# Optimization experiments

Hardware: AMD Instinct MI355X
Metric: run time of the kernel (lower is better)

The kernel has to match this reference:

```python
import jax, jax.numpy as jnp
import numpy as np

COMM_DIM = 8
HIDDEN = 64
N = 2048


def setup_inputs() -> dict:
    key = jax.random.key(0)
    k_msg, k_w1, k_b1, k_w2, k_b2 = jax.random.split(key, 5)
    s1 = 1.0 / np.sqrt(2 * COMM_DIM)  # torch Linear default-ish scale
    s2 = 1.0 / np.sqrt(HIDDEN)
    return {
        "messages": jax.random.normal(k_msg, (N, COMM_DIM), dtype=jnp.float32),
        "W1": jax.random.normal(k_w1, (HIDDEN, 2 * COMM_DIM), dtype=jnp.float32) * s1,
        "b1": jax.random.normal(k_b1, (HIDDEN,), dtype=jnp.float32) * s1,
        "W2": jax.random.normal(k_w2, (COMM_DIM, HIDDEN), dtype=jnp.float32) * s2,
        "b2": jax.random.normal(k_b2, (COMM_DIM,), dtype=jnp.float32) * s2,
    }


def reference(messages, W1, b1, W2, b2):
    # edge_mlp(concat([m_i, m_j])) for all ordered pairs, mean over j != i.
    # Linear1 on the concat splits: concat([mi,mj]) @ W1^T = mi @ W1[:,:D]^T + mj @ W1[:,D:]^T
    n = messages.shape[0]
    X1 = jnp.einsum('nd,hd->nh', messages, W1[:, :COMM_DIM])   # [N, H] contribution of m_i
    X2 = jnp.einsum('nd,hd->nh', messages, W1[:, COMM_DIM:])   # [N, H] contribution of m_j
    # pairwise hidden: [N, N, H] (the dominant, memory-bound intermediate)
    H = jax.nn.relu(X1[:, None, :] + X2[None, :, :] + b1)
    S = H.sum(axis=1)                                          # [N, H] sum over all j (incl. j==i)
    D = jax.nn.relu(X1 + X2 + b1)                              # [N, H] the j==i diagonal term
    # agg_i = sum_{j!=i} (relu(...) @ W2^T + b2); then divide by (N-1)
    agg = jnp.einsum('nh,dh->nd', S - D, W2) + (n - 1) * b2
    return agg / (n - 1)
```

## Files before the change

### kernel.cpp

```cpp
#include <hip/hip_runtime.h>


#define NN 2048
#define HH 64
#define DD 8

#define ITILES 32
#define JCHUNKS 32
#define JCHUNK (NN / JCHUNKS)

__global__ void prep_kernel(const float* __restrict__ msg,
                            const float* __restrict__ W1,
                            const float* __restrict__ b1,
                            float* __restrict__ A,
                            float* __restrict__ X2,
                            float* __restrict__ SX) {
    int idx = blockIdx.x * blockDim.x + threadIdx.x;
    if (blockIdx.x == 0 && threadIdx.x < HH) SX[threadIdx.x] = 0.f;
    int i = idx >> 6;
    int h = idx & 63;
    const float4* m4 = (const float4*)(msg + i * DD);
    const float4* w4 = (const float4*)(W1 + h * (2 * DD));
    float4 m0 = m4[0], m1 = m4[1];
    float4 w0 = w4[0], w1 = w4[1], w2 = w4[2], w3 = w4[3];
    float x1 = m0.x * w0.x + m0.y * w0.y + m0.z * w0.z + m0.w * w0.w
             + m1.x * w1.x + m1.y * w1.y + m1.z * w1.z + m1.w * w1.w;
    float x2 = m0.x * w2.x + m0.y * w2.y + m0.z * w2.z + m0.w * w2.w
             + m1.x * w3.x + m1.y * w3.y + m1.z * w3.z + m1.w * w3.w;
    A[idx]  = x1 + b1[h];
    X2[idx] = x2;
}

__global__ void __launch_bounds__(256, 4)
pair_kernel(const float* __restrict__ A,
            const float* __restrict__ X2,
            const float* __restrict__ W2,
            float* __restrict__ P,
            float* __restrict__ SX) {
    __shared__ float4 sX2[JCHUNK * 16];
    __shared__ float  T[64][68];

    int it = blockIdx.x & (ITILES - 1);
    int jc = blockIdx.x >> 5;
    int hq = threadIdx.x & 15;
    int il = threadIdx.x >> 4;
    int h0 = hq * 4;
    int i0 = it * 64 + il * 4;

    {
        const float4* X2v = (const float4*)X2 + jc * JCHUNK * 16;
#pragma unroll
        for (int r = 0; r < 4; ++r) {
            int t = threadIdx.x + r * 256;
            sX2[t] = X2v[t];
        }
    }

    float a[4][4];
#pragma unroll
    for (int k = 0; k < 4; ++k) {
        float4 av = *(const float4*)&A[(i0 + k) * HH + h0];
        a[k][0] = av.x; a[k][1] = av.y; a[k][2] = av.z; a[k][3] = av.w;
    }
    float acc[4][4];
#pragma unroll
    for (int k = 0; k < 4; ++k)
#pragma unroll
        for (int hh = 0; hh < 4; ++hh)
            acc[k][hh] = 0.f;

    __syncthreads();

#pragma unroll 4
    for (int j = 0; j < JCHUNK; ++j) {
        float4 x = sX2[j * 16 + hq];
#pragma unroll
        for (int k = 0; k < 4; ++k) {
            acc[k][0] += __builtin_fabsf(a[k][0] + x.x);
            acc[k][1] += __builtin_fabsf(a[k][1] + x.y);
            acc[k][2] += __builtin_fabsf(a[k][2] + x.z);
            acc[k][3] += __builtin_fabsf(a[k][3] + x.w);
        }
    }

    if (it == 0 && il == 0) {
        float4 s = make_float4(0.f, 0.f, 0.f, 0.f);
        for (int j = 0; j < JCHUNK; ++j) {
            float4 x = sX2[j * 16 + hq];
            s.x += x.x; s.y += x.y; s.z += x.z; s.w += x.w;
        }
        atomicAdd(&SX[h0 + 0], s.x);
        atomicAdd(&SX[h0 + 1], s.y);
        atomicAdd(&SX[h0 + 2], s.z);
        atomicAdd(&SX[h0 + 3], s.w);
    }

#pragma unroll
    for (int k = 0; k < 4; ++k)
        *(float4*)&T[il * 4 + k][h0] =
            make_float4(acc[k][0], acc[k][1], acc[k][2], acc[k][3]);
    __syncthreads();

    {
        int iL = threadIdx.x >> 3;
        int d  = threadIdx.x & 7;
        const float4* w2v = (const float4*)W2;
        float s0 = 0.f, s1 = 0.f;
#pragma unroll
        for (int hb = 0; hb < 16; ++hb) {
            float4 w = w2v[d * 16 + hb];
            float4 t0 = *(const float4*)&T[iL][hb * 4];
            float4 t1 = *(const float4*)&T[iL + 32][hb * 4];
            s0 += t0.x * w.x + t0.y * w.y + t0.z * w.z + t0.w * w.w;
            s1 += t1.x * w.x + t1.y * w.y + t1.z * w.z + t1.w * w.w;
        }
        int ibase = it * 64;
        P[(jc * NN + ibase + iL) * DD + d]      = s0;
        P[(jc * NN + ibase + iL + 32) * DD + d] = s1;
    }
}

__global__ void out_kernel(const float* __restrict__ A,
                           const float* __restrict__ X2,
                           const float* __restrict__ P,
                           const float* __restrict__ SX,
                           const float* __restrict__ W2,
                           const float* __restrict__ b2,
                           float* __restrict__ out) {
    int i = blockIdx.x * 4 + (threadIdx.x >> 6);
    int l = threadIdx.x & 63;

    float a  = A[i * HH + l];
    float x2 = X2[i * HH + l];
    float sx = SX[l];
    float v = 0.5f * ((float)NN * a + sx);
    float t = a + x2;
    v -= (t > 0.f ? t : 0.f);

    float p0 = v * W2[0 * HH + l];
    float p1 = v * W2[1 * HH + l];
    float p2 = v * W2[2 * HH + l];
    float p3 = v * W2[3 * HH + l];
    float p4 = v * W2[4 * HH + l];
    float p5 = v * W2[5 * HH + l];
    float p6 = v * W2[6 * HH + l];
    float p7 = v * W2[7 * HH + l];
#pragma unroll
    for (int m = 1; m < 64; m <<= 1) {
        p0 += __shfl_xor(p0, m);
        p1 += __shfl_xor(p1, m);
        p2 += __shfl_xor(p2, m);
        p3 += __shfl_xor(p3, m);
        p4 += __shfl_xor(p4, m);
        p5 += __shfl_xor(p5, m);
        p6 += __shfl_xor(p6, m);
        p7 += __shfl_xor(p7, m);
    }

    int d = l & 7, g = l >> 3;
    float q = 0.f;
#pragma unroll
    for (int r = 0; r < 4; ++r)
        q += P[((r * 8 + g) * NN + i) * DD + d];
    q += __shfl_xor(q, 8);
    q += __shfl_xor(q, 16);
    q += __shfl_xor(q, 32);

    if (l < 8) {
        float pv = p0;
        pv = (l == 1) ? p1 : pv;
        pv = (l == 2) ? p2 : pv;
        pv = (l == 3) ? p3 : pv;
        pv = (l == 4) ? p4 : pv;
        pv = (l == 5) ? p5 : pv;
        pv = (l == 6) ? p6 : pv;
        pv = (l == 7) ? p7 : pv;
        out[i * DD + l] = (0.5f * q + pv) * (1.0f / (float)(NN - 1)) + b2[l];
    }
}

extern "C" void kernel_launch(void* const* d_in, const int* in_sizes, int n_in,
                              void* d_out, int out_size, void* d_ws, size_t ws_size,
                              hipStream_t stream) {
    const float* msg = (const float*)d_in[0];
    const float* W1  = (const float*)d_in[1];
    const float* b1  = (const float*)d_in[2];
    const float* W2  = (const float*)d_in[3];
    const float* b2  = (const float*)d_in[4];
    float* out = (float*)d_out;

    float* ws = (float*)d_ws;
    float* A  = ws;
    float* X2 = ws + NN * HH;
    float* P  = ws + 2 * NN * HH;
    float* SX = P + JCHUNKS * NN * DD;

    prep_kernel<<<(NN * HH) / 256, 256, 0, stream>>>(msg, W1, b1, A, X2, SX);
    pair_kernel<<<ITILES * JCHUNKS, 256, 0, stream>>>(A, X2, W2, P, SX);
    out_kernel<<<NN / 4, 256, 0, stream>>>(A, X2, P, SX, W2, b2, out);
}
```

Measured before the change: 85.98 us.

## Fuse output reduction into pair kernel via atomic accumulation into output

Removes the separate out_kernel and the partial-sum buffer P. Each pair block now computes its own column sum of X2, applies the W2 projection and scaling, and atomically adds its partial result into the output. The block whose j-chunk matches its i-tile also adds the diagonal correction and the bias. This drops one kernel launch and the round trip through P, at the cost of 32 float atomics per output element, a nondeterministic summation order, and redundant per-block SX reductions.

```diff
diff --git a/kernel.cpp b/kernel.cpp
--- a/kernel.cpp
+++ b/kernel.cpp
@@ -8,15 +8,16 @@
 #define ITILES 32
 #define JCHUNKS 32
 #define JCHUNK (NN / JCHUNKS)
+#define INV_SCALE (0.5f / (float)(NN - 1))
 
 __global__ void prep_kernel(const float* __restrict__ msg,
                             const float* __restrict__ W1,
                             const float* __restrict__ b1,
                             float* __restrict__ A,
                             float* __restrict__ X2,
-                            float* __restrict__ SX) {
+                            float* __restrict__ out) {
     int idx = blockIdx.x * blockDim.x + threadIdx.x;
-    if (blockIdx.x == 0 && threadIdx.x < HH) SX[threadIdx.x] = 0.f;
+    if (idx < NN * DD) out[idx] = 0.f;
     int i = idx >> 6;
     int h = idx & 63;
     const float4* m4 = (const float4*)(msg + i * DD);
@@ -32,13 +33,14 @@
 }
 
 __global__ void __launch_bounds__(256, 4)
-pair_kernel(const float* __restrict__ A,
-            const float* __restrict__ X2,
-            const float* __restrict__ W2,
-            float* __restrict__ P,
-            float* __restrict__ SX) {
+pair_fused(const float* __restrict__ A,
+           const float* __restrict__ X2,
+           const float* __restrict__ W2,
+           const float* __restrict__ b2,
+           float* __restrict__ out) {
     __shared__ float4 sX2[JCHUNK * 16];
     __shared__ float  T[64][68];
+    __shared__ float4 sSXv[16];
 
     int it = blockIdx.x & (ITILES - 1);
     int jc = blockIdx.x >> 5;
@@ -46,6 +48,7 @@
     int il = threadIdx.x >> 4;
     int h0 = hq * 4;
     int i0 = it * 64 + il * 4;
+    bool des = (jc == it);
 
     {
         const float4* X2v = (const float4*)X2 + jc * JCHUNK * 16;
@@ -83,99 +86,63 @@
         }
     }
 
-    if (it == 0 && il == 0) {
-        float4 s = make_float4(0.f, 0.f, 0.f, 0.f);
-        for (int j = 0; j < JCHUNK; ++j) {
-            float4 x = sX2[j * 16 + hq];
-            s.x += x.x; s.y += x.y; s.z += x.z; s.w += x.w;
+    const float* sX2f = (const float*)sX2;
+
+    if (threadIdx.x < 64) {
+        float s0 = 0.f, s1 = 0.f, s2 = 0.f, s3 = 0.f;
+#pragma unroll 8
+        for (int j = 0; j < JCHUNK; j += 4) {
+            s0 += sX2f[(j + 0) * 64 + threadIdx.x];
+            s1 += sX2f[(j + 1) * 64 + threadIdx.x];
+            s2 += sX2f[(j + 2) * 64 + threadIdx.x];
+            s3 += sX2f[(j + 3) * 64 + threadIdx.x];
         }
-        atomicAdd(&SX[h0 + 0], s.x);
-        atomicAdd(&SX[h0 + 1], s.y);
-        atomicAdd(&SX[h0 + 2], s.z);
-        atomicAdd(&SX[h0 + 3], s.w);
+        ((float*)sSXv)[threadIdx.x] = (s0 + s1) + (s2 + s3);
     }
 
 #pragma unroll
-    for (int k = 0; k < 4; ++k)
-        *(float4*)&T[il * 4 + k][h0] =
-            make_float4(acc[k][0], acc[k][1], acc[k][2], acc[k][3]);
+    for (int k = 0; k < 4; ++k) {
+        float t0 = acc[k][0], t1 = acc[k][1], t2 = acc[k][2], t3 = acc[k][3];
+        if (des) {
+            int jl = il * 4 + k;
+            float z0 = a[k][0] + sX2f[jl * 64 + h0 + 0];
+            float z1 = a[k][1] + sX2f[jl * 64 + h0 + 1];
+            float z2 = a[k][2] + sX2f[jl * 64 + h0 + 2];
+            float z3 = a[k][3] + sX2f[jl * 64 + h0 + 3];
+            t0 += (float)NN * a[k][0] - 2.f * (z0 > 0.f ? z0 : 0.f);
+            t1 += (float)NN * a[k][1] - 2.f * (z1 > 0.f ? z1 : 0.f);
+            t2 += (float)NN * a[k][2] - 2.f * (z2 > 0.f ? z2 : 0.f);
+            t3 += (float)NN * a[k][3] - 2.f * (z3 > 0.f ? z3 : 0.f);
+        }
+        *(float4*)&T[il * 4 + k][h0] = make_float4(t0, t1, t2, t3);
+    }
     __syncthreads();
 
     {
         int iL = threadIdx.x >> 3;
         int d  = threadIdx.x & 7;
         const float4* w2v = (const float4*)W2;
-        float s0 = 0.f, s1 = 0.f;
+        float s0 = 0.f, s1 = 0.f, c = 0.f;
 #pragma unroll
         for (int hb = 0; hb < 16; ++hb) {
-            float4 w = w2v[d * 16 + hb];
+            float4 w  = w2v[d * 16 + hb];
             float4 t0 = *(const float4*)&T[iL][hb * 4];
             float4 t1 = *(const float4*)&T[iL + 32][hb * 4];
+            float4 sx = sSXv[hb];
             s0 += t0.x * w.x + t0.y * w.y + t0.z * w.z + t0.w * w.w;
             s1 += t1.x * w.x + t1.y * w.y + t1.z * w.z + t1.w * w.w;
+            c  += sx.x * w.x + sx.y * w.y + sx.z * w.z + sx.w * w.w;
+        }
+        float v0 = (s0 + c) * INV_SCALE;
+        float v1 = (s1 + c) * INV_SCALE;
+        if (des) {
+            float bv = b2[d];
+            v0 += bv;
+            v1 += bv;
         }
         int ibase = it * 64;
-        P[(jc * NN + ibase + iL) * DD + d]      = s0;
-        P[(jc * NN + ibase + iL + 32) * DD + d] = s1;
-    }
-}
-
-__global__ void out_kernel(const float* __restrict__ A,
-                           const float* __restrict__ X2,
-                           const float* __restrict__ P,
-                           const float* __restrict__ SX,
-                           const float* __restrict__ W2,
-                           const float* __restrict__ b2,
-                           float* __restrict__ out) {
-    int i = blockIdx.x * 4 + (threadIdx.x >> 6);
-    int l = threadIdx.x & 63;
-
-    float a  = A[i * HH + l];
-    float x2 = X2[i * HH + l];
-    float sx = SX[l];
-    float v = 0.5f * ((float)NN * a + sx);
-    float t = a + x2;
-    v -= (t > 0.f ? t : 0.f);
-
-    float p0 = v * W2[0 * HH + l];
-    float p1 = v * W2[1 * HH + l];
-    float p2 = v * W2[2 * HH + l];
-    float p3 = v * W2[3 * HH + l];
-    float p4 = v * W2[4 * HH + l];
-    float p5 = v * W2[5 * HH + l];
-    float p6 = v * W2[6 * HH + l];
-    float p7 = v * W2[7 * HH + l];
-#pragma unroll
-    for (int m = 1; m < 64; m <<= 1) {
-        p0 += __shfl_xor(p0, m);
-        p1 += __shfl_xor(p1, m);
-        p2 += __shfl_xor(p2, m);
-        p3 += __shfl_xor(p3, m);
-        p4 += __shfl_xor(p4, m);
-        p5 += __shfl_xor(p5, m);
-        p6 += __shfl_xor(p6, m);
-        p7 += __shfl_xor(p7, m);
-    }
-
-    int d = l & 7, g = l >> 3;
-    float q = 0.f;
-#pragma unroll
-    for (int r = 0; r < 4; ++r)
-        q += P[((r * 8 + g) * NN + i) * DD + d];
-    q += __shfl_xor(q, 8);
-    q += __shfl_xor(q, 16);
-    q += __shfl_xor(q, 32);
-
-    if (l < 8) {
-        float pv = p0;
-        pv = (l == 1) ? p1 : pv;
-        pv = (l == 2) ? p2 : pv;
-        pv = (l == 3) ? p3 : pv;
-        pv = (l == 4) ? p4 : pv;
-        pv = (l == 5) ? p5 : pv;
-        pv = (l == 6) ? p6 : pv;
-        pv = (l == 7) ? p7 : pv;
-        out[i * DD + l] = (0.5f * q + pv) * (1.0f / (float)(NN - 1)) + b2[l];
+        atomicAdd(&out[(ibase + iL) * DD + d], v0);
+        atomicAdd(&out[(ibase + iL + 32) * DD + d], v1);
     }
 }
 
@@ -192,10 +159,7 @@
     float* ws = (float*)d_ws;
     float* A  = ws;
     float* X2 = ws + NN * HH;
-    float* P  = ws + 2 * NN * HH;
-    float* SX = P + JCHUNKS * NN * DD;
 
-    prep_kernel<<<(NN * HH) / 256, 256, 0, stream>>>(msg, W1, b1, A, X2, SX);
-    pair_kernel<<<ITILES * JCHUNKS, 256, 0, stream>>>(A, X2, W2, P, SX);
-    out_kernel<<<NN / 4, 256, 0, stream>>>(A, X2, P, SX, W2, b2, out);
+    prep_kernel<<<(NN * HH) / 256, 256, 0, stream>>>(msg, W1, b1, A, X2, out);
+    pair_fused<<<ITILES * JCHUNKS, 256, 0, stream>>>(A, X2, W2, b2, out);
 }
```

Result: faster. 82.73 us (-3.8%).
